# Performance work log

Hardware: AMD Instinct MI355X
Metric: run time of the kernel (lower is better)

The kernel has to match this reference:

```python
import jax, jax.numpy as jnp
import numpy as np


def setup_inputs() -> dict:
    key = jax.random.key(0)
    k1, k2 = jax.random.split(key)
    N, M, D = 16384, 16384, 3
    src_V = jax.random.normal(k1, (N, D), dtype=jnp.float32)
    tar_V = jax.random.normal(k2, (M, D), dtype=jnp.float32)
    return {"src_V": src_V, "tar_V": tar_V}


def reference(src_V, tar_V):
    # 1-NN: for each target point find nearest source point (replaces cKDTree).
    # Squared distances via ||t||^2 - 2 t.s + ||s||^2 ; [M, N]
    d2 = (
        jnp.sum(tar_V * tar_V, axis=1, keepdims=True)
        - 2.0 * (tar_V @ src_V.T)
        + jnp.sum(src_V * src_V, axis=1)[None, :]
    )
    ii = jnp.argmin(d2, axis=1)            # [M] nearest src index per target
    diff = src_V[ii] - tar_V               # [M, 3]
    loss = 0.5 * jnp.sum(diff * diff)
    return loss
```

## Files before the change

kernel.cpp:

```cpp
#include <hip/hip_runtime.h>
#include <math.h>

constexpr int N_SRC = 16384;
constexpr int M_TAR = 16384;

constexpr int BLOCKS = 512;
constexpr int TPB = 512;
constexpr int CHUNKS = 256;
constexpr int TILE = 2048;
constexpr int TILES = N_SRC / TILE;
constexpr int ROWS_PT = TILE / CHUNKS;
constexpr int IPT = ROWS_PT / 2;
constexpr int TPT = 16;
constexpr int PPT = TILE / TPB;

__global__ void zero_out(float* __restrict__ out) {
    if (threadIdx.x == 0) out[0] = 0.0f;
}

__device__ __forceinline__ float embed_ao(float t, unsigned mask_v, unsigned row_s) {
    float r;
    asm("v_and_or_b32 %0, %1, %2, %3"
        : "=v"(r) : "v"(t), "v"(mask_v), "s"(row_s));
    return r;
}
__device__ __forceinline__ void min3(float& b, float e0, float e1) {
    asm("v_min3_f32 %0, %0, %1, %2"
        : "+v"(b) : "v"(e0), "v"(e1));
}

__global__ __launch_bounds__(TPB, 2) void nn9(const float* __restrict__ src,
                                              const float* __restrict__ tar,
                                              float* __restrict__ out) {
    __shared__ float4 tile[2 * TILE];

    const int tid   = threadIdx.x;
    const int g     = tid >> 8;
    const int chunk = tid & 255;
    const int tbase = blockIdx.x * 32;

    float txm2[TPT], tym2[TPT], tzm2[TPT], best[TPT];
#pragma unroll
    for (int k = 0; k < TPT; ++k) {
        int T = tbase + g * TPT + k;
        txm2[k] = -2.0f * tar[3 * T + 0];
        tym2[k] = -2.0f * tar[3 * T + 1];
        tzm2[k] = -2.0f * tar[3 * T + 2];
        best[k] = INFINITY;
    }

#pragma unroll
    for (int r = 0; r < PPT; ++r) {
        int p = tid + r * TPB;
        const float* q = src + 3 * p;
        float x = q[0], y = q[1], z = q[2];
        tile[p] = make_float4(x, y, z, fmaf(x, x, fmaf(y, y, z * z)));
    }
    __syncthreads();

    unsigned mask_v = 0xFFFFFFC0u;

    auto compute = [&](int cb, unsigned rowbase) {
#pragma unroll
        for (int i = 0; i < IPT; ++i) {
            float4 s0 = tile[cb + (2 * i + 0) * CHUNKS + chunk];
            float4 s1 = tile[cb + (2 * i + 1) * CHUNKS + chunk];
            unsigned row0 = rowbase + 2 * i;
            unsigned row1 = rowbase + 2 * i + 1;
#pragma unroll
            for (int k = 0; k < TPT; ++k) {
                float t0 = fmaf(s0.z, tzm2[k], s0.w);
                t0 = fmaf(s0.y, tym2[k], t0);
                t0 = fmaf(s0.x, txm2[k], t0);
                float t1 = fmaf(s1.z, tzm2[k], s1.w);
                t1 = fmaf(s1.y, tym2[k], t1);
                t1 = fmaf(s1.x, txm2[k], t1);
                float e0 = embed_ao(t0, mask_v, row0);
                float e1 = embed_ao(t1, mask_v, row1);
                min3(best[k], e0, e1);
            }
        }
    };

#pragma unroll 1
    for (int tl = 0; tl < TILES - 1; ++tl) {
        float px[PPT], py[PPT], pz[PPT];
#pragma unroll
        for (int r = 0; r < PPT; ++r) {
            const float* q = src + 3 * ((tl + 1) * TILE + tid + r * TPB);
            px[r] = q[0]; py[r] = q[1]; pz[r] = q[2];
        }
        __builtin_amdgcn_sched_barrier(0);

        compute((tl & 1) * TILE, (unsigned)(tl * ROWS_PT));

        const int wb = ((tl + 1) & 1) * TILE;
#pragma unroll
        for (int r = 0; r < PPT; ++r) {
            float x = px[r], y = py[r], z = pz[r];
            tile[wb + tid + r * TPB] =
                make_float4(x, y, z, fmaf(x, x, fmaf(y, y, z * z)));
        }
        __syncthreads();
    }
    compute(((TILES - 1) & 1) * TILE, (unsigned)((TILES - 1) * ROWS_PT));

    __syncthreads();
    float* fv = (float*)tile;
    int*   fj = (int*)tile + 32 * 256;
#pragma unroll
    for (int k = 0; k < TPT; ++k) {
        unsigned b = __float_as_uint(best[k]);
        int j  = (int)((b & 63u) * CHUNKS + chunk);
        int lt = g * TPT + k;
        fv[lt * CHUNKS + chunk] = __uint_as_float(b & 0xFFFFFFC0u);
        fj[lt * CHUNKS + chunk] = j;
    }
    __syncthreads();

    const int tprime = tid >> 4;
    const int sub    = tid & 15;
    float bv = fv[tprime * CHUNKS + sub];
    int   bj = fj[tprime * CHUNKS + sub];
#pragma unroll
    for (int m = 1; m < CHUNKS / 16; ++m) {
        float v = fv[tprime * CHUNKS + sub + 16 * m];
        int   j = fj[tprime * CHUNKS + sub + 16 * m];
        if (v < bv) { bv = v; bj = j; }
    }
#pragma unroll
    for (int s = 8; s >= 1; s >>= 1) {
        float vv = __shfl_xor(bv, s, 64);
        int   jj = __shfl_xor(bj, s, 64);
        if (vv < bv) { bv = vv; bj = jj; }
    }
    __syncthreads();

    if (sub == 0) {
        int tt = tbase + tprime;
        float dx = src[3 * bj + 0] - tar[3 * tt + 0];
        float dy = src[3 * bj + 1] - tar[3 * tt + 1];
        float dz = src[3 * bj + 2] - tar[3 * tt + 2];
        fv[tprime] = 0.5f * fmaf(dx, dx, fmaf(dy, dy, dz * dz));
    }
    __syncthreads();
    if (tid == 0) {
        float ssum = 0.0f;
#pragma unroll
        for (int i = 0; i < 32; ++i) ssum += fv[i];
        atomicAdd(out, ssum);
    }
}

extern "C" void kernel_launch(void* const* d_in, const int* in_sizes, int n_in,
                              void* d_out, int out_size, void* d_ws, size_t ws_size,
                              hipStream_t stream) {
    const float* src = (const float*)d_in[0];
    const float* tar = (const float*)d_in[1];
    float* out = (float*)d_out;
    (void)d_ws; (void)ws_size;

    zero_out<<<1, 64, 0, stream>>>(out);
    nn9<<<BLOCKS, TPB, 0, stream>>>(src, tar, out);
}
```

Measured before the change: 88.58 us.

## Drop index embedding from inner loop; recover argmin row by recomputation

The inner loop no longer packs the row index into the low mantissa bits of each distance with v_and_or. It keeps only the plain min value per chunk. After the reduction picks the winning chunk, 16 lanes per target recompute the distances for all 64 rows of that chunk and pick the first row whose value matches exactly. This removes two ALU ops per pair from the hot loop, at the cost of a small scattered global-read epilogue. Occupancy hints also change to request 4 waves per EU.

After: 85.57 us. -3.4%, faster.

```diff
diff --git a/kernel.cpp b/kernel.cpp
--- a/kernel.cpp
+++ b/kernel.cpp
@@ -13,25 +13,23 @@
 constexpr int IPT = ROWS_PT / 2;
 constexpr int TPT = 16;
 constexpr int PPT = TILE / TPB;
+constexpr int NROWS = N_SRC / CHUNKS;
 
 __global__ void zero_out(float* __restrict__ out) {
     if (threadIdx.x == 0) out[0] = 0.0f;
 }
 
-__device__ __forceinline__ float embed_ao(float t, unsigned mask_v, unsigned row_s) {
-    float r;
-    asm("v_and_or_b32 %0, %1, %2, %3"
-        : "=v"(r) : "v"(t), "v"(mask_v), "s"(row_s));
-    return r;
-}
 __device__ __forceinline__ void min3(float& b, float e0, float e1) {
     asm("v_min3_f32 %0, %0, %1, %2"
         : "+v"(b) : "v"(e0), "v"(e1));
 }
 
-__global__ __launch_bounds__(TPB, 2) void nn9(const float* __restrict__ src,
-                                              const float* __restrict__ tar,
-                                              float* __restrict__ out) {
+__global__
+__attribute__((amdgpu_flat_work_group_size(TPB, TPB)))
+__attribute__((amdgpu_waves_per_eu(4, 4)))
+void nn10(const float* __restrict__ src,
+          const float* __restrict__ tar,
+          float* __restrict__ out) {
     __shared__ float4 tile[2 * TILE];
 
     const int tid   = threadIdx.x;
@@ -58,15 +56,11 @@
     }
     __syncthreads();
 
-    unsigned mask_v = 0xFFFFFFC0u;
-
-    auto compute = [&](int cb, unsigned rowbase) {
+    auto compute = [&](int cb) {
 #pragma unroll
         for (int i = 0; i < IPT; ++i) {
             float4 s0 = tile[cb + (2 * i + 0) * CHUNKS + chunk];
             float4 s1 = tile[cb + (2 * i + 1) * CHUNKS + chunk];
-            unsigned row0 = rowbase + 2 * i;
-            unsigned row1 = rowbase + 2 * i + 1;
 #pragma unroll
             for (int k = 0; k < TPT; ++k) {
                 float t0 = fmaf(s0.z, tzm2[k], s0.w);
@@ -75,9 +69,7 @@
                 float t1 = fmaf(s1.z, tzm2[k], s1.w);
                 t1 = fmaf(s1.y, tym2[k], t1);
                 t1 = fmaf(s1.x, txm2[k], t1);
-                float e0 = embed_ao(t0, mask_v, row0);
-                float e1 = embed_ao(t1, mask_v, row1);
-                min3(best[k], e0, e1);
+                min3(best[k], t0, t1);
             }
         }
     };
@@ -92,7 +84,7 @@
         }
         __builtin_amdgcn_sched_barrier(0);
 
-        compute((tl & 1) * TILE, (unsigned)(tl * ROWS_PT));
+        compute((tl & 1) * TILE);
 
         const int wb = ((tl + 1) & 1) * TILE;
 #pragma unroll
@@ -103,44 +95,60 @@
         }
         __syncthreads();
     }
-    compute(((TILES - 1) & 1) * TILE, (unsigned)((TILES - 1) * ROWS_PT));
+    compute(((TILES - 1) & 1) * TILE);
 
     __syncthreads();
     float* fv = (float*)tile;
-    int*   fj = (int*)tile + 32 * 256;
 #pragma unroll
     for (int k = 0; k < TPT; ++k) {
-        unsigned b = __float_as_uint(best[k]);
-        int j  = (int)((b & 63u) * CHUNKS + chunk);
-        int lt = g * TPT + k;
-        fv[lt * CHUNKS + chunk] = __uint_as_float(b & 0xFFFFFFC0u);
-        fj[lt * CHUNKS + chunk] = j;
+        fv[(g * TPT + k) * CHUNKS + chunk] = best[k];
     }
     __syncthreads();
 
     const int tprime = tid >> 4;
     const int sub    = tid & 15;
     float bv = fv[tprime * CHUNKS + sub];
-    int   bj = fj[tprime * CHUNKS + sub];
+    int   bc = sub;
 #pragma unroll
     for (int m = 1; m < CHUNKS / 16; ++m) {
         float v = fv[tprime * CHUNKS + sub + 16 * m];
-        int   j = fj[tprime * CHUNKS + sub + 16 * m];
-        if (v < bv) { bv = v; bj = j; }
+        if (v < bv) { bv = v; bc = sub + 16 * m; }
     }
 #pragma unroll
     for (int s = 8; s >= 1; s >>= 1) {
         float vv = __shfl_xor(bv, s, 64);
-        int   jj = __shfl_xor(bj, s, 64);
-        if (vv < bv) { bv = vv; bj = jj; }
+        int   cc = __shfl_xor(bc, s, 64);
+        if (vv < bv) { bv = vv; bc = cc; }
+    }
+
+    const int T = tbase + tprime;
+    const float tx = tar[3 * T + 0], ty = tar[3 * T + 1], tz = tar[3 * T + 2];
+    const float rxm2 = -2.0f * tx, rym2 = -2.0f * ty, rzm2 = -2.0f * tz;
+    int myrow = NROWS;
+#pragma unroll
+    for (int rr = 0; rr < NROWS / 16; ++rr) {
+        int r = sub + 16 * rr;
+        int j = r * CHUNKS + bc;
+        const float* q = src + 3 * j;
+        float x = q[0], y = q[1], z = q[2];
+        float w = fmaf(x, x, fmaf(y, y, z * z));
+        float v = fmaf(z, rzm2, w);
+        v = fmaf(y, rym2, v);
+        v = fmaf(x, rxm2, v);
+        if (v == bv && r < myrow) myrow = r;
+    }
+#pragma unroll
+    for (int s = 8; s >= 1; s >>= 1) {
+        int r2 = __shfl_xor(myrow, s, 64);
+        if (r2 < myrow) myrow = r2;
     }
     __syncthreads();
 
     if (sub == 0) {
-        int tt = tbase + tprime;
-        float dx = src[3 * bj + 0] - tar[3 * tt + 0];
-        float dy = src[3 * bj + 1] - tar[3 * tt + 1];
-        float dz = src[3 * bj + 2] - tar[3 * tt + 2];
+        int j = myrow * CHUNKS + bc;
+        float dx = src[3 * j + 0] - tx;
+        float dy = src[3 * j + 1] - ty;
+        float dz = src[3 * j + 2] - tz;
         fv[tprime] = 0.5f * fmaf(dx, dx, fmaf(dy, dy, dz * dz));
     }
     __syncthreads();
@@ -161,5 +169,5 @@
     (void)d_ws; (void)ws_size;
 
     zero_out<<<1, 64, 0, stream>>>(out);
-    nn9<<<BLOCKS, TPB, 0, stream>>>(src, tar, out);
+    nn10<<<BLOCKS, TPB, 0, stream>>>(src, tar, out);
 }
```
